# Kernel tuning notes

Hardware: AMD Instinct MI355X
Metric: run time of the kernel (lower is better)

Reference implementation:

```python
import jax, jax.numpy as jnp
import numpy as np

D = 2048  # filter_dim
B = 4096  # tokens per TTT step


def setup_inputs() -> dict:
    key = jax.random.key(0)
    ks = jax.random.split(key, 8)
    s = 1.0 / np.sqrt(D)  # kaiming-ish scale so activations stay O(1)
    return {
        "src": jax.random.normal(ks[0], (B, D), jnp.float32),
        "theta_k": jax.random.normal(ks[1], (D, D), jnp.float32) * s,
        "theta_q": jax.random.normal(ks[2], (D, D), jnp.float32) * s,
        "theta_v": jax.random.normal(ks[3], (D, D), jnp.float32) * s,
        "W": jax.random.normal(ks[4], (D, D), jnp.float32) * s,
        "b": jnp.zeros((D,), jnp.float32),
        "lr_w": jax.random.uniform(ks[5], (D, D), jnp.float32) * 0.1,
        "lr_b": jax.random.uniform(ks[6], (D,), jnp.float32) * 0.1,
    }


def reference(src, theta_k, theta_q, theta_v, W, b, lr_w, lr_b):
    # Projections: src is [B, D], thetas are [D, D]
    train_view = src @ theta_k           # [B, D]
    label_view = src @ theta_v           # [B, D]
    test_view = src @ theta_q            # [B, D]

    target = label_view - train_view     # reconstruction target
    pred = train_view @ W.T + b          # nn.Linear(train_view)
    err = pred - target                  # [B, D]

    # Analytic grads of MSELoss (mean over B*D elements) wrt W ([D,D]) and b ([D])
    n = err.size  # B * D (static)
    coef = 2.0 / n
    gW = coef * (err.T @ train_view)     # [D, D], matches w.weight layout
    gb = coef * jnp.sum(err, axis=0)     # [D]

    # Per-element learning-rate SGD step (the in-place parameter rewrite)
    W_new = W - lr_w * gW
    b_new = b - lr_b * gb

    # Query with updated weights + residual
    z = test_view @ W_new.T + b_new + test_view
    return z
```

## Files before the change

### kernel.cpp

```cpp
#include <hip/hip_runtime.h>
#include <hip/hip_bf16.h>
#include <hip/hip_fp8.h>
#include <stdint.h>

#define D_DIM 2048
#define B_TOK 4096
#define COEF (2.0f / 8388608.0f)

typedef __bf16 bf16x8 __attribute__((ext_vector_type(8)));
typedef float  f32x4  __attribute__((ext_vector_type(4)));
typedef int    i32x8  __attribute__((ext_vector_type(8)));
typedef unsigned short u16x8 __attribute__((ext_vector_type(8)));

__device__ __forceinline__ unsigned short f2bf(float f) {
  return __builtin_bit_cast(unsigned short, (__bf16)f);
}
__device__ __forceinline__ float bf2f(unsigned short u) {
  return (float)__builtin_bit_cast(__bf16, u);
}
__device__ __forceinline__ unsigned char f2f8(float f) {
  __hip_fp8_e4m3 v(f);
  return v.__x;
}

__device__ __forceinline__ void async16(const void* g, void* l) {
  __builtin_amdgcn_global_load_lds(
      (__attribute__((address_space(1))) void*)(g),
      (__attribute__((address_space(3))) void*)(l),
      16, 0, 0);
}

__device__ __forceinline__ void gemm_core_256(const unsigned short* __restrict__ Ablk,
                                              const unsigned short* __restrict__ Bblk,
                                              const int lda, const int ldb, const int KC,
                                              unsigned short* As, unsigned short* Bs,
                                              f32x4 acc[4][4]) {
  const int tid  = threadIdx.x;
  const int lane = tid & 63;
  const int wv   = tid >> 6;
  const int wm   = wv >> 1;
  const int wn   = wv & 1;
  const int t    = lane & 15;
  const int quad = lane >> 4;
  const int lrow = lane >> 3;
  const int kq   = lane & 7;
  const int kqs  = kq ^ lrow;

  const int nk = KC >> 6;

  auto stage = [&](int buf, int kt) {
    const int k0 = kt << 6;
    unsigned short* Ad = As + buf * 16384;
    unsigned short* Bd = Bs + buf * 8192;
#pragma unroll
    for (int l = 0; l < 4; ++l) {
      const int seg = wv * 4 + l;
      const int r   = seg * 8 + lrow;
      async16(Ablk + (size_t)r * lda + k0 + kqs * 8, Ad + seg * 512);
    }
#pragma unroll
    for (int l = 0; l < 2; ++l) {
      const int seg = wv * 2 + l;
      const int r   = seg * 8 + lrow;
      async16(Bblk + (size_t)r * ldb + k0 + kqs * 8, Bd + seg * 512);
    }
  };

  stage(0, 0);
  if (nk > 1) stage(1, 1);
  int cur = 0, nxt = 2;
  for (int kt = 0; kt < nk; ++kt) {
    if (kt + 1 < nk) asm volatile("s_waitcnt vmcnt(6)" ::: "memory");
    else             asm volatile("s_waitcnt vmcnt(0)" ::: "memory");
    __builtin_amdgcn_s_barrier();
    __builtin_amdgcn_sched_barrier(0);
    if (kt + 2 < nk) stage(nxt, kt + 2);
    __builtin_amdgcn_sched_barrier(0);
    const unsigned short* Ac = As + cur * 16384;
    const unsigned short* Bc = Bs + cur * 8192;
#pragma unroll
    for (int s = 0; s < 2; ++s) {
      bf16x8 af[4], bfr[4];
#pragma unroll
      for (int i = 0; i < 4; ++i) {
        const int rm = wm * 64 + i * 16 + t;
        af[i]  = *(const bf16x8*)(Ac + rm * 64 + (((s << 2) + quad) ^ (rm & 7)) * 8);
        const int rn = wn * 64 + i * 16 + t;
        bfr[i] = *(const bf16x8*)(Bc + rn * 64 + (((s << 2) + quad) ^ (rn & 7)) * 8);
      }
      __builtin_amdgcn_s_setprio(1);
#pragma unroll
      for (int i = 0; i < 4; ++i)
#pragma unroll
        for (int j = 0; j < 4; ++j)
          acc[i][j] = __builtin_amdgcn_mfma_f32_16x16x32_bf16(af[i], bfr[j], acc[i][j], 0, 0, 0);
      __builtin_amdgcn_s_setprio(0);
    }
    cur = (cur == 2) ? 0 : cur + 1;
    nxt = (nxt == 2) ? 0 : nxt + 1;
  }
}

#define GEMM_PROLOGUE256(AP, BP, LDAv, LDBv, KCv)                              \
  __shared__ __align__(16) unsigned short As[3 * 16384];                       \
  __shared__ __align__(16) unsigned short Bs[3 * 8192];                        \
  const int lin = blockIdx.y * 16 + blockIdx.x;                                \
  const int swz = (lin & 7) * 32 + (lin >> 3);                                 \
  const int bx = swz & 15, by = swz >> 4;                                      \
  const unsigned short* Ablk = (AP) + (size_t)by * 256 * (LDAv);               \
  const unsigned short* Bblk = (BP) + (size_t)bx * 128 * (LDBv);               \
  f32x4 acc[4][4];                                                             \
  _Pragma("unroll") for (int i = 0; i < 4; ++i)                                \
  _Pragma("unroll") for (int j = 0; j < 4; ++j)                                \
      acc[i][j] = (f32x4){0.f, 0.f, 0.f, 0.f};                                 \
  gemm_core_256(Ablk, Bblk, (LDAv), (LDBv), (KCv), As, Bs, acc);               \
  const int lane = threadIdx.x & 63;                                           \
  const int wv = threadIdx.x >> 6;                                             \
  const int wm = wv >> 1, wn = wv & 1;                                         \
  const int t = lane & 15, quad = lane >> 4;                                   \
  const int gm_base = by * 256 + wm * 64;                                      \
  const int gn_base = bx * 128 + wn * 64;

__device__ __forceinline__ void gemm_core_f8(const unsigned char* __restrict__ Ablk,
                                             const unsigned char* __restrict__ Bblk,
                                             const int lda, const int ldb, const int KC,
                                             unsigned char* As, unsigned char* Bs,
                                             f32x4 acc[4][4]) {
  const int tid  = threadIdx.x;
  const int lane = tid & 63;
  const int wv   = tid >> 6;
  const int wm   = wv & 1, wn = wv >> 1;
  const int t    = lane & 15;
  const int quad = lane >> 4;
  const int lrow = lane >> 3;
  const int kq   = lane & 7;
  const int kqs  = kq ^ lrow;

  const int nk = KC >> 7;
  for (int kt = 0; kt < nk; ++kt) {
    const int k0 = kt << 7;
#pragma unroll
    for (int l = 0; l < 4; ++l) {
      const int seg = wv * 4 + l;
      const int r   = seg * 8 + lrow;
      async16(Ablk + (size_t)r * lda + k0 + kqs * 16, As + seg * 1024);
      async16(Bblk + (size_t)r * ldb + k0 + kqs * 16, Bs + seg * 1024);
    }
    __syncthreads();
    i32x8 af[4];
#pragma unroll
    for (int i = 0; i < 4; ++i) {
      const int rm = wm * 64 + i * 16 + t;
      const unsigned char* base = As + rm * 128;
      const int x = rm & 7;
      const uint4 lo = *(const uint4*)(base + (((quad << 1)    ) ^ x) * 16);
      const uint4 hi = *(const uint4*)(base + (((quad << 1) | 1) ^ x) * 16);
      af[i] = (i32x8){(int)lo.x, (int)lo.y, (int)lo.z, (int)lo.w,
                      (int)hi.x, (int)hi.y, (int)hi.z, (int)hi.w};
    }
#pragma unroll
    for (int j = 0; j < 4; ++j) {
      const int rn = wn * 64 + j * 16 + t;
      const unsigned char* base = Bs + rn * 128;
      const int x = rn & 7;
      const uint4 lo = *(const uint4*)(base + (((quad << 1)    ) ^ x) * 16);
      const uint4 hi = *(const uint4*)(base + (((quad << 1) | 1) ^ x) * 16);
      const i32x8 bq = (i32x8){(int)lo.x, (int)lo.y, (int)lo.z, (int)lo.w,
                               (int)hi.x, (int)hi.y, (int)hi.z, (int)hi.w};
#pragma unroll
      for (int i = 0; i < 4; ++i)
        acc[i][j] = __builtin_amdgcn_mfma_scale_f32_16x16x128_f8f6f4(
            af[i], bq, acc[i][j], 0, 0, 0, 127, 0, 127);
    }
    __syncthreads();
  }
}

#define GEMM8_PROLOGUE(AP, BP, LDAv, LDBv, KCv)                                \
  __shared__ __align__(16) unsigned char As8[128 * 128];                       \
  __shared__ __align__(16) unsigned char Bs8[128 * 128];                       \
  const unsigned char* Ablk = (AP) + (size_t)blockIdx.y * 128 * (LDAv);        \
  const unsigned char* Bblk = (BP) + (size_t)blockIdx.x * 128 * (LDBv);        \
  f32x4 acc[4][4];                                                             \
  _Pragma("unroll") for (int i = 0; i < 4; ++i)                                \
  _Pragma("unroll") for (int j = 0; j < 4; ++j)                                \
      acc[i][j] = (f32x4){0.f, 0.f, 0.f, 0.f};                                 \
  gemm_core_f8(Ablk, Bblk, (LDAv), (LDBv), (KCv), As8, Bs8, acc);              \
  const int lane = threadIdx.x & 63;                                           \
  const int wv = threadIdx.x >> 6;                                             \
  const int wm = wv & 1, wn = wv >> 1;                                         \
  const int t = lane & 15, quad = lane >> 4;                                   \
  const int gm_base = blockIdx.y * 128 + wm * 64;                              \
  const int gn_base = blockIdx.x * 128 + wn * 64;

__global__ __launch_bounds__(256) void gemm_train_f8(
    const unsigned char* __restrict__ srcA,
    const unsigned char* __restrict__ thkT8,
    unsigned char* __restrict__ src_cat_f8,
    unsigned char* __restrict__ trainT8) {
  GEMM8_PROLOGUE(srcA, thkT8, 4096, 2048, 2048)
  unsigned char* scr = ((wv >> 1) ? Bs8 : As8) + (wv & 1) * 2304;
#pragma unroll
  for (int p = 0; p < 2; ++p) {
#pragma unroll
    for (int jl = 0; jl < 2; ++jl) {
      const int j = p * 2 + jl;
      const int gn = gn_base + j * 16 + t;
#pragma unroll
      for (int i = 0; i < 4; ++i) {
        const int gm0 = gm_base + i * 16 + quad * 4;
        uchar4 pk = make_uchar4(f2f8(acc[i][j][0]), f2f8(acc[i][j][1]),
                                f2f8(acc[i][j][2]), f2f8(acc[i][j][3]));
        src_cat_f8[(size_t)(gm0 + 0) * 4096 + gn] = pk.x;
        src_cat_f8[(size_t)(gm0 + 1) * 4096 + gn] = pk.y;
        src_cat_f8[(size_t)(gm0 + 2) * 4096 + gn] = pk.z;
        src_cat_f8[(size_t)(gm0 + 3) * 4096 + gn] = pk.w;
        *(uchar4*)(scr + (jl * 16 + t) * 72 + i * 16 + quad * 4) = pk;
      }
    }
    __syncthreads();
    const int row = lane >> 3, chunk = lane & 7;
#pragma unroll
    for (int q = 0; q < 4; ++q) {
      const int rr = q * 8 + row;
      const uint2 v = *(const uint2*)(scr + rr * 72 + chunk * 8);
      *(uint2*)(trainT8 + (size_t)(gn_base + p * 32 + rr) * B_TOK + gm_base + chunk * 8) = v;
    }
    __syncthreads();
  }
}

__global__ __launch_bounds__(512, 2) void gemm_test(
    const unsigned short* __restrict__ src_bf,
    const unsigned short* __restrict__ thqT,
    unsigned short* __restrict__ testv) {
  GEMM_PROLOGUE256(src_bf, thqT, 2048, 2048, 2048)
#pragma unroll
  for (int i = 0; i < 4; ++i) {
#pragma unroll
    for (int j = 0; j < 4; ++j) {
      const int gm0 = gm_base + i * 16 + quad * 4;
      const int gn  = gn_base + j * 16 + t;
#pragma unroll
      for (int r = 0; r < 4; ++r)
        testv[(size_t)(gm0 + r) * D_DIM + gn] = f2bf(acc[i][j][r]);
    }
  }
}

__global__ __launch_bounds__(256) void gemm_err_f8(
    const unsigned char* __restrict__ src_cat_f8,
    const unsigned char* __restrict__ Wcat_f8,
    const float* __restrict__ bvec,
    unsigned char* __restrict__ errT8,
    float* __restrict__ gb) {
  GEMM8_PROLOGUE(src_cat_f8, Wcat_f8, 4096, 4096, 4096)
  unsigned char* scr = ((wv >> 1) ? Bs8 : As8) + (wv & 1) * 2304;
#pragma unroll
  for (int p = 0; p < 2; ++p) {
#pragma unroll
    for (int jl = 0; jl < 2; ++jl) {
      const int j = p * 2 + jl;
      const int gn = gn_base + j * 16 + t;
      const float bias = bvec[gn];
      float cs = 0.f;
#pragma unroll
      for (int i = 0; i < 4; ++i) {
        const float e0 = acc[i][j][0] + bias, e1 = acc[i][j][1] + bias;
        const float e2 = acc[i][j][2] + bias, e3 = acc[i][j][3] + bias;
        *(uchar4*)(scr + (jl * 16 + t) * 72 + i * 16 + quad * 4) =
            make_uchar4(f2f8(e0), f2f8(e1), f2f8(e2), f2f8(e3));
        cs += e0 + e1 + e2 + e3;
      }
      cs += __shfl_xor(cs, 16);
      cs += __shfl_xor(cs, 32);
      if (quad == 0) atomicAdd(&gb[gn], cs);
    }
    __syncthreads();
    const int row = lane >> 3, chunk = lane & 7;
#pragma unroll
    for (int q = 0; q < 4; ++q) {
      const int rr = q * 8 + row;
      const uint2 v = *(const uint2*)(scr + rr * 72 + chunk * 8);
      *(uint2*)(errT8 + (size_t)(gn_base + p * 32 + rr) * B_TOK + gm_base + chunk * 8) = v;
    }
    __syncthreads();
  }
}

__global__ __launch_bounds__(256) void gemm_gw_f8(
    const unsigned char* __restrict__ errT8,
    const unsigned char* __restrict__ trainT8,
    float* __restrict__ P0, float* __restrict__ P1) {
  const int z = blockIdx.z;
  const unsigned char* Abase = errT8 + z * 2048;
  const unsigned char* Bbase = trainT8 + z * 2048;
  GEMM8_PROLOGUE(Abase, Bbase, B_TOK, B_TOK, 2048)
  float* P = (z == 0) ? P0 : P1;
#pragma unroll
  for (int i = 0; i < 4; ++i) {
#pragma unroll
    for (int j = 0; j < 4; ++j) {
      const int gm0 = gm_base + i * 16 + quad * 4;
      const int gn  = gn_base + j * 16 + t;
#pragma unroll
      for (int r = 0; r < 4; ++r)
        P[(size_t)(gm0 + r) * D_DIM + gn] = acc[i][j][r];
    }
  }
}

__global__ __launch_bounds__(256) void wnew_reduce(
    const float* __restrict__ P0, const float* __restrict__ P1,
    const float* __restrict__ W, const float* __restrict__ lr_w,
    unsigned short* __restrict__ Wnew) {
  const int i = blockIdx.x * 256 + threadIdx.x;
  const float4 p0 = ((const float4*)P0)[i];
  const float4 p1 = ((const float4*)P1)[i];
  const float4 w  = ((const float4*)W)[i];
  const float4 l  = ((const float4*)lr_w)[i];
  ((ushort4*)Wnew)[i] = make_ushort4(
      f2bf(w.x - l.x * (COEF * (p0.x + p1.x))),
      f2bf(w.y - l.y * (COEF * (p0.y + p1.y))),
      f2bf(w.z - l.z * (COEF * (p0.z + p1.z))),
      f2bf(w.w - l.w * (COEF * (p0.w + p1.w))));
}

__global__ __launch_bounds__(512, 2) void gemm_out(
    const unsigned short* __restrict__ testv,
    const unsigned short* __restrict__ Wnew,
    const float* __restrict__ bvec,
    const float* __restrict__ lr_b,
    const float* __restrict__ gb,
    float* __restrict__ out) {
  GEMM_PROLOGUE256(testv, Wnew, 2048, 2048, 2048)
#pragma unroll
  for (int j = 0; j < 4; ++j) {
    const int gn = gn_base + j * 16 + t;
    const float bias = bvec[gn] - lr_b[gn] * (COEF * gb[gn]);
#pragma unroll
    for (int i = 0; i < 4; ++i) {
      const int gm0 = gm_base + i * 16 + quad * 4;
#pragma unroll
      for (int r = 0; r < 4; ++r) {
        const size_t idx = (size_t)(gm0 + r) * D_DIM + gn;
        out[idx] = acc[i][j][r] + bias + bf2f(testv[idx]);
      }
    }
  }
}

__global__ __launch_bounds__(256) void cvt_all(const float* __restrict__ src,
                                               const float* __restrict__ W,
                                               unsigned short* __restrict__ src_bf,
                                               unsigned char* __restrict__ src_cat_f8,
                                               unsigned char* __restrict__ Wcat_f8,
                                               float* __restrict__ gb) {
  const int i = blockIdx.x * 256 + threadIdx.x;
  if (i < 512) ((float4*)gb)[i] = (float4){0.f, 0.f, 0.f, 0.f};
  if (i < 2097152) {
    const int m = i >> 9, c = i & 511;
    const float4 v = ((const float4*)src)[i];
    ((ushort4*)src_bf)[i] = make_ushort4(f2bf(v.x), f2bf(v.y), f2bf(v.z), f2bf(v.w));
    *(uchar4*)(src_cat_f8 + (size_t)m * 4096 + 2048 + c * 4) =
        make_uchar4(f2f8(v.x), f2f8(v.y), f2f8(v.z), f2f8(v.w));
  } else {
    const int j = i - 2097152;
    const int n = j >> 9, c = j & 511;
    const float4 v = ((const float4*)W)[j];
    *(uchar4*)(Wcat_f8 + (size_t)n * 4096 + c * 4) =
        make_uchar4(f2f8(v.x), f2f8(v.y), f2f8(v.z), f2f8(v.w));
  }
}

__global__ __launch_bounds__(256) void tcvt(
    const float* __restrict__ thk, const float* __restrict__ thq,
    const float* __restrict__ thv,
    unsigned char* __restrict__ thkT8, unsigned short* __restrict__ thqT,
    unsigned char* __restrict__ Wcat_f8) {
  __shared__ float tile[32][33];
  const int z = blockIdx.z;
  const int bx = blockIdx.x * 32, by = blockIdx.y * 32;
  const int tx = threadIdx.x & 31, ty = threadIdx.x >> 5;
#pragma unroll
  for (int l = 0; l < 4; ++l) {
    const int r = ty + l * 8;
    const size_t idx = (size_t)(by + r) * D_DIM + bx + tx;
    tile[r][tx] = (z == 0) ? thk[idx] : (z == 1) ? thq[idx] : (thk[idx] - thv[idx]);
  }
  __syncthreads();
#pragma unroll
  for (int l = 0; l < 4; ++l) {
    const int r = ty + l * 8;
    if (z == 0)
      thkT8[(size_t)(bx + r) * 2048 + by + tx] = f2f8(tile[tx][r]);
    else if (z == 1)
      thqT[(size_t)(bx + r) * 2048 + by + tx] = f2bf(tile[tx][r]);
    else
      Wcat_f8[(size_t)(bx + r) * 4096 + 2048 + by + tx] = f2f8(tile[tx][r]);
  }
}

extern "C" void kernel_launch(void* const* d_in, const int* in_sizes, int n_in,
                              void* d_out, int out_size, void* d_ws, size_t ws_size,
                              hipStream_t stream) {
  const float* src = (const float*)d_in[0];
  const float* thk = (const float*)d_in[1];
  const float* thq = (const float*)d_in[2];
  const float* thv = (const float*)d_in[3];
  const float* W   = (const float*)d_in[4];
  const float* bv  = (const float*)d_in[5];
  const float* lrw = (const float*)d_in[6];
  const float* lrb = (const float*)d_in[7];
  float* out = (float*)d_out;

  char* ws = (char*)d_ws;
  const size_t MB = 1024 * 1024;
  unsigned short* src_bf     = (unsigned short*)(ws + 0);
  unsigned char*  src_cat_f8 = (unsigned char*)(ws + 16 * MB);
  unsigned char*  Wcat_f8    = (unsigned char*)(ws + 32 * MB);
  unsigned char*  thkT8      = (unsigned char*)(ws + 40 * MB);
  unsigned short* thqT       = (unsigned short*)(ws + 44 * MB);
  unsigned char*  trainT8    = (unsigned char*)(ws + 52 * MB);
  unsigned short* testv      = (unsigned short*)(ws + 60 * MB);
  unsigned char*  errT8      = (unsigned char*)(ws + 76 * MB);
  unsigned short* WnewBf     = (unsigned short*)(ws + 84 * MB);
  float*          P0         = (float*)(ws + 92 * MB);
  float*          P1         = (float*)(ws + 108 * MB);
  float*          gb         = (float*)(ws + 124 * MB);

  cvt_all<<<12288, 256, 0, stream>>>(src, W, src_bf, src_cat_f8, Wcat_f8, gb);
  tcvt<<<dim3(64, 64, 3), 256, 0, stream>>>(thk, thq, thv, thkT8, thqT, Wcat_f8);

  gemm_train_f8<<<dim3(16, 32), 256, 0, stream>>>(src_cat_f8 + 2048, thkT8,
                                                  src_cat_f8, trainT8);
  gemm_test<<<dim3(16, 16), 512, 0, stream>>>(src_bf, thqT, testv);
  gemm_err_f8<<<dim3(16, 32), 256, 0, stream>>>(src_cat_f8, Wcat_f8, bv, errT8, gb);
  gemm_gw_f8<<<dim3(16, 16, 2), 256, 0, stream>>>(errT8, trainT8, P0, P1);
  wnew_reduce<<<4096, 256, 0, stream>>>(P0, P1, W, lrw, WnewBf);
  gemm_out<<<dim3(16, 16), 512, 0, stream>>>(testv, WnewBf, bv, lrb, gb, out);
}
```

Measured before the change: 357.6 us.

## Split K-tile into two phases interleaving prefetch loads with MFMA clusters

Restructures the GEMM main loop into two half-tile phases. Each phase reads its LDS fragments, issues half of the next-next tile's global-to-LDS loads, then hits a barrier and runs its MFMA cluster, in a ping-pong style schedule. The aim is to spread memory issue across the iteration and line up waves so loads and MFMAs overlap better. The cost is extra block-level barriers per K step, which could stall waves, and a finer-grained vmcnt accounting that has to stay correct.

```diff
diff --git a/kernel.cpp b/kernel.cpp
--- a/kernel.cpp
+++ b/kernel.cpp
@@ -10,7 +10,6 @@
 typedef __bf16 bf16x8 __attribute__((ext_vector_type(8)));
 typedef float  f32x4  __attribute__((ext_vector_type(4)));
 typedef int    i32x8  __attribute__((ext_vector_type(8)));
-typedef unsigned short u16x8 __attribute__((ext_vector_type(8)));
 
 __device__ __forceinline__ unsigned short f2bf(float f) {
   return __builtin_bit_cast(unsigned short, (__bf16)f);
@@ -48,56 +47,87 @@
 
   const int nk = KC >> 6;
 
-  auto stage = [&](int buf, int kt) {
+  auto stageA2 = [&](int buf, int kt, int l0) {
     const int k0 = kt << 6;
     unsigned short* Ad = As + buf * 16384;
-    unsigned short* Bd = Bs + buf * 8192;
-#pragma unroll
-    for (int l = 0; l < 4; ++l) {
+#pragma unroll
+    for (int l = l0; l < l0 + 2; ++l) {
       const int seg = wv * 4 + l;
       const int r   = seg * 8 + lrow;
       async16(Ablk + (size_t)r * lda + k0 + kqs * 8, Ad + seg * 512);
     }
-#pragma unroll
-    for (int l = 0; l < 2; ++l) {
-      const int seg = wv * 2 + l;
-      const int r   = seg * 8 + lrow;
-      async16(Bblk + (size_t)r * ldb + k0 + kqs * 8, Bd + seg * 512);
-    }
   };
-
-  stage(0, 0);
-  if (nk > 1) stage(1, 1);
-  int cur = 0, nxt = 2;
+  auto stageB1 = [&](int buf, int kt, int l) {
+    const int k0 = kt << 6;
+    unsigned short* Bd = Bs + buf * 8192;
+    const int seg = wv * 2 + l;
+    const int r   = seg * 8 + lrow;
+    async16(Bblk + (size_t)r * ldb + k0 + kqs * 8, Bd + seg * 512);
+  };
+
+  stageA2(0, 0, 0); stageA2(0, 0, 2); stageB1(0, 0, 0); stageB1(0, 0, 1);
+  if (nk > 1) { stageA2(1, 1, 0); stageA2(1, 1, 2); stageB1(1, 1, 0); stageB1(1, 1, 1); }
+  if (nk > 1) asm volatile("s_waitcnt vmcnt(6)" ::: "memory");
+  else        asm volatile("s_waitcnt vmcnt(0)" ::: "memory");
+  __builtin_amdgcn_s_barrier();
+
+  int cur = 0;
   for (int kt = 0; kt < nk; ++kt) {
-    if (kt + 1 < nk) asm volatile("s_waitcnt vmcnt(6)" ::: "memory");
-    else             asm volatile("s_waitcnt vmcnt(0)" ::: "memory");
-    __builtin_amdgcn_s_barrier();
-    __builtin_amdgcn_sched_barrier(0);
-    if (kt + 2 < nk) stage(nxt, kt + 2);
-    __builtin_amdgcn_sched_barrier(0);
     const unsigned short* Ac = As + cur * 16384;
     const unsigned short* Bc = Bs + cur * 8192;
-#pragma unroll
-    for (int s = 0; s < 2; ++s) {
-      bf16x8 af[4], bfr[4];
-#pragma unroll
-      for (int i = 0; i < 4; ++i) {
-        const int rm = wm * 64 + i * 16 + t;
-        af[i]  = *(const bf16x8*)(Ac + rm * 64 + (((s << 2) + quad) ^ (rm & 7)) * 8);
-        const int rn = wn * 64 + i * 16 + t;
-        bfr[i] = *(const bf16x8*)(Bc + rn * 64 + (((s << 2) + quad) ^ (rn & 7)) * 8);
-      }
-      __builtin_amdgcn_s_setprio(1);
-#pragma unroll
-      for (int i = 0; i < 4; ++i)
-#pragma unroll
-        for (int j = 0; j < 4; ++j)
-          acc[i][j] = __builtin_amdgcn_mfma_f32_16x16x32_bf16(af[i], bfr[j], acc[i][j], 0, 0, 0);
-      __builtin_amdgcn_s_setprio(0);
-    }
+    const int nb = (cur >= 1) ? cur - 1 : 2;
+    const bool pf = (kt + 2 < nk);
+
+    bf16x8 af[4], bfr[4];
+#pragma unroll
+    for (int i = 0; i < 4; ++i) {
+      const int rm = wm * 64 + i * 16 + t;
+      af[i]  = *(const bf16x8*)(Ac + rm * 64 + ((quad) ^ (rm & 7)) * 8);
+      const int rn = wn * 64 + i * 16 + t;
+      bfr[i] = *(const bf16x8*)(Bc + rn * 64 + ((quad) ^ (rn & 7)) * 8);
+    }
+    __builtin_amdgcn_sched_barrier(0);
+    if (pf) { stageA2(nb, kt + 2, 0); stageB1(nb, kt + 2, 0); }
+    __builtin_amdgcn_sched_barrier(0);
+    __builtin_amdgcn_s_barrier();
+    asm volatile("s_waitcnt lgkmcnt(0)" ::: "memory");
+    __builtin_amdgcn_sched_barrier(0);
+    __builtin_amdgcn_s_setprio(1);
+#pragma unroll
+    for (int i = 0; i < 4; ++i)
+#pragma unroll
+      for (int j = 0; j < 4; ++j)
+        acc[i][j] = __builtin_amdgcn_mfma_f32_16x16x32_bf16(af[i], bfr[j], acc[i][j], 0, 0, 0);
+    __builtin_amdgcn_s_setprio(0);
+    __builtin_amdgcn_sched_barrier(0);
+    __builtin_amdgcn_s_barrier();
+
+#pragma unroll
+    for (int i = 0; i < 4; ++i) {
+      const int rm = wm * 64 + i * 16 + t;
+      af[i]  = *(const bf16x8*)(Ac + rm * 64 + ((4 + quad) ^ (rm & 7)) * 8);
+      const int rn = wn * 64 + i * 16 + t;
+      bfr[i] = *(const bf16x8*)(Bc + rn * 64 + ((4 + quad) ^ (rn & 7)) * 8);
+    }
+    __builtin_amdgcn_sched_barrier(0);
+    if (pf) { stageA2(nb, kt + 2, 2); stageB1(nb, kt + 2, 1); }
+    __builtin_amdgcn_sched_barrier(0);
+    if (pf)               asm volatile("s_waitcnt vmcnt(6)" ::: "memory");
+    else if (kt + 1 < nk) asm volatile("s_waitcnt vmcnt(0)" ::: "memory");
+    __builtin_amdgcn_s_barrier();
+    asm volatile("s_waitcnt lgkmcnt(0)" ::: "memory");
+    __builtin_amdgcn_sched_barrier(0);
+    __builtin_amdgcn_s_setprio(1);
+#pragma unroll
+    for (int i = 0; i < 4; ++i)
+#pragma unroll
+      for (int j = 0; j < 4; ++j)
+        acc[i][j] = __builtin_amdgcn_mfma_f32_16x16x32_bf16(af[i], bfr[j], acc[i][j], 0, 0, 0);
+    __builtin_amdgcn_s_setprio(0);
+    __builtin_amdgcn_sched_barrier(0);
+    __builtin_amdgcn_s_barrier();
+
     cur = (cur == 2) ? 0 : cur + 1;
-    nxt = (nxt == 2) ? 0 : nxt + 1;
   }
 }
 
```

Result: faster. 341.0 us (-4.6%).
